# Kernel tuning notes

Measured on AMD Instinct MI355X. Metric: run time of the kernel, lower is better.

The kernel has to match this reference:

```python
import jax, jax.numpy as jnp
import numpy as np


def swiglu(g, u):
    return jax.nn.silu(g) * u


def setup_inputs() -> dict:
    key = jax.random.key(0)
    ks = jax.random.split(key, 10)
    D, H, E, HS = 2048, 512, 32, 1024
    B, S = 1, 2048
    s = 0.02
    return {
        "x": jax.random.normal(ks[0], (B, S, D), jnp.float32),
        "gate_w": jax.random.normal(ks[1], (E, D), jnp.float32) * s,
        "expert_bias": jnp.zeros((E,), jnp.float32),
        "wg": jax.random.normal(ks[2], (E, D, H), jnp.float32) * s,
        "wu": jax.random.normal(ks[3], (E, D, H), jnp.float32) * s,
        "wd": jax.random.normal(ks[4], (E, H, D), jnp.float32) * s,
        "sg": jax.random.normal(ks[5], (D, HS), jnp.float32) * s,
        "su": jax.random.normal(ks[6], (D, HS), jnp.float32) * s,
        "sd": jax.random.normal(ks[7], (HS, D), jnp.float32) * s,
        "coef_w": jax.random.normal(ks[8], (2, D), jnp.float32) * s,
        "coef_b": jnp.zeros((2,), jnp.float32),
        "top_k": 4,
    }


def reference(x, gate_w, expert_bias, wg, wu, wd, sg, su, sd, coef_w, coef_b, top_k):
    # --- sigmoid router with bias-adjusted top-k selection ---
    logits = jnp.einsum("bsd,ed->bse", x, gate_w)            # [B,S,E]
    routing = jax.nn.sigmoid(logits.astype(jnp.float32))
    biased = routing + expert_bias[None, None, :]
    _, inds = jax.lax.top_k(biased, top_k)                    # [B,S,k]
    scores = jnp.take_along_axis(routing, inds, axis=-1)      # gather UNbiased weights
    scores = scores / (jnp.sum(scores, axis=-1, keepdims=True) + 1e-20)  # norm_topk_prob
    scores = scores.astype(x.dtype)

    # --- SwitchGLU experts: dense per-expert SwiGLU, then gather top-k outputs ---
    h = jnp.einsum("bsd,edh->bseh", x, wg)                    # [B,S,E,H]
    u = jnp.einsum("bsd,edh->bseh", x, wu)
    y_all = jnp.einsum("bseh,ehd->bsed", swiglu(h, u), wd)    # [B,S,E,D]
    expert_out = jnp.take_along_axis(
        y_all, inds[..., None], axis=2)                        # [B,S,k,D]
    y_experts = jnp.sum(expert_out * scores[..., None], axis=-2)  # [B,S,D]

    # --- shared expert + learned 2-way mixing coefficient ---
    shared = swiglu(x @ sg, x @ su) @ sd                      # [B,S,D]
    coef = jax.nn.softmax(jnp.einsum("bsd,cd->bsc", x, coef_w) + coef_b, axis=-1)
    return y_experts * coef[..., :1] + shared * coef[..., 1:]
```

## Files before the change

### kernel.cpp

```cpp
#include <hip/hip_runtime.h>
#include <hip/hip_bf16.h>
#include <stdint.h>

#define S_TOK   2048
#define DMODEL  2048
#define HEXP    512
#define NEXP    32
#define HSH     1024
#define NPAIR   (S_TOK * 4)
#define NT128   96
#define NT64    160

#define M128_NT  0
#define M128_TE  1
#define M128_TP0 (1 + NT128)
#define M128_TM  (1 + 2 * NT128)
#define M64_NT   (1 + 3 * NT128)
#define M64_TE   (M64_NT + 1)
#define M64_TP0  (M64_NT + 1 + NT64)
#define M64_TM   (M64_NT + 1 + 2 * NT64)
#define META_SIZE (M64_NT + 1 + 3 * NT64)

typedef short  s16x8 __attribute__((ext_vector_type(8)));
typedef __bf16 b16x8 __attribute__((ext_vector_type(8)));
typedef float  f32x4 __attribute__((ext_vector_type(4)));

__device__ __forceinline__ f32x4 mfma16x16x32(s16x8 a, s16x8 b, f32x4 c) {
    return __builtin_amdgcn_mfma_f32_16x16x32_bf16(
        __builtin_bit_cast(b16x8, a), __builtin_bit_cast(b16x8, b), c, 0, 0, 0);
}

__device__ __forceinline__ unsigned short f2bf(float f) {
    union { float f; unsigned int u; } v; v.f = f;
    unsigned int u = v.u;
    return (unsigned short)((u + 0x7FFFu + ((u >> 16) & 1u)) >> 16);
}

__device__ __forceinline__ float bf2f(unsigned short b) {
    union { unsigned int u; float f; } v; v.u = ((unsigned int)b) << 16;
    return v.f;
}

__device__ __forceinline__ void gload16(const unsigned short* g, unsigned short* l) {
    __builtin_amdgcn_global_load_lds(
        (const __attribute__((address_space(1))) void*)(uintptr_t)g,
        (__attribute__((address_space(3))) void*)(uintptr_t)l, 16, 0, 0);
}

__global__ __launch_bounds__(256)
void router_kernel(const float* __restrict__ x, const float* __restrict__ gate_w,
                   const float* __restrict__ expert_bias,
                   const float* __restrict__ coef_w, const float* __restrict__ coef_b,
                   int* __restrict__ inds, float* __restrict__ scores,
                   float* __restrict__ coefo)
{
    const int t = blockIdx.x;
    const int tid = threadIdx.x;
    const int lane = tid & 63;
    const int wave = tid >> 6;
    const float* xr = x + (size_t)t * DMODEL;

    float xv[32];
#pragma unroll
    for (int j = 0; j < 32; ++j) xv[j] = xr[lane + 64 * j];

    __shared__ float s_logits[NEXP];
    __shared__ float s_coef[2];

    for (int i = 0; i < 8; ++i) {
        const int e = wave * 8 + i;
        const float* wr = gate_w + (size_t)e * DMODEL;
        float p = 0.f;
#pragma unroll
        for (int j = 0; j < 32; ++j) p += xv[j] * wr[lane + 64 * j];
#pragma unroll
        for (int o = 32; o > 0; o >>= 1) p += __shfl_xor(p, o);
        if (lane == 0) s_logits[e] = p;
    }
    if (wave == 0) {
        for (int c = 0; c < 2; ++c) {
            const float* wr = coef_w + (size_t)c * DMODEL;
            float p = 0.f;
#pragma unroll
            for (int j = 0; j < 32; ++j) p += xv[j] * wr[lane + 64 * j];
#pragma unroll
            for (int o = 32; o > 0; o >>= 1) p += __shfl_xor(p, o);
            if (lane == 0) s_coef[c] = p;
        }
    }
    __syncthreads();
    if (tid == 0) {
        float routing[NEXP], biased[NEXP];
        for (int e = 0; e < NEXP; ++e) {
            const float r = 1.f / (1.f + expf(-s_logits[e]));
            routing[e] = r;
            biased[e] = r + expert_bias[e];
        }
        int sel[4]; float sc[4]; float ssum = 0.f;
        for (int k = 0; k < 4; ++k) {
            int best = 0; float bv = -1e30f;
            for (int e = 0; e < NEXP; ++e)
                if (biased[e] > bv) { bv = biased[e]; best = e; }
            sel[k] = best; sc[k] = routing[best]; ssum += sc[k];
            biased[best] = -1e30f;
        }
        const float inv = 1.f / (ssum + 1e-20f);
        for (int k = 0; k < 4; ++k) {
            inds[t * 4 + k] = sel[k];
            scores[t * 4 + k] = sc[k] * inv;
        }
        const float l0 = s_coef[0] + coef_b[0];
        const float l1 = s_coef[1] + coef_b[1];
        const float m = fmaxf(l0, l1);
        const float e0 = expf(l0 - m), e1 = expf(l1 - m);
        coefo[t * 2 + 0] = e0 / (e0 + e1);
        coefo[t * 2 + 1] = e1 / (e0 + e1);
    }
}

__global__ __launch_bounds__(256)
void xcast_kernel(const float* __restrict__ x, unsigned short* __restrict__ xb)
{
    const int i = (blockIdx.x * 256 + threadIdx.x) * 4;
    const float4 v = *reinterpret_cast<const float4*>(x + i);
    ushort4 o;
    o.x = f2bf(v.x); o.y = f2bf(v.y); o.z = f2bf(v.z); o.w = f2bf(v.w);
    *reinterpret_cast<ushort4*>(xb + i) = o;
}

__global__ __launch_bounds__(256)
void tconv_kernel(const float* __restrict__ src, unsigned short* __restrict__ dst,
                  const int K, const int N)
{
    __shared__ unsigned short T[64][80];
    const size_t boff = (size_t)blockIdx.z * K * N;
    const float* s = src + boff;
    unsigned short* d = dst + boff;
    const int n0 = blockIdx.x * 64, k0 = blockIdx.y * 64;
    const int tid = threadIdx.x;

    const int n4 = (tid & 15) * 4;
    const int kr = tid >> 4;
#pragma unroll
    for (int i = 0; i < 4; ++i) {
        const int k = kr + i * 16;
        const float4 v = *reinterpret_cast<const float4*>(s + (size_t)(k0 + k) * N + n0 + n4);
        T[n4 + 0][k] = f2bf(v.x);
        T[n4 + 1][k] = f2bf(v.y);
        T[n4 + 2][k] = f2bf(v.z);
        T[n4 + 3][k] = f2bf(v.w);
    }
    __syncthreads();
    const int nw = tid >> 2;
    const int kc = (tid & 3) * 16;
    uint4* o = reinterpret_cast<uint4*>(d + (size_t)(n0 + nw) * K + k0 + kc);
    o[0] = *reinterpret_cast<const uint4*>(&T[nw][kc]);
    o[1] = *reinterpret_cast<const uint4*>(&T[nw][kc + 8]);
}

__global__ __launch_bounds__(1024)
void group_kernel(const int* __restrict__ inds, const float* __restrict__ scores,
                  int* __restrict__ meta, int* __restrict__ pair_token,
                  float* __restrict__ pair_score, int* __restrict__ tok_pos)
{
    __shared__ int cnt[NEXP];
    __shared__ int off_s[NEXP];
    __shared__ int cur[NEXP];
    const int tid = threadIdx.x;
    if (tid < NEXP) cnt[tid] = 0;
    __syncthreads();
    for (int i = tid; i < NPAIR; i += 1024) atomicAdd(&cnt[inds[i]], 1);
    __syncthreads();
    if (tid == 0) {
        int run = 0, nt1 = 0, nt2 = 0;
        for (int e = 0; e < NEXP; ++e) {
            off_s[e] = run;
            const int c = cnt[e];
            for (int m0 = 0; m0 < c; m0 += 128) {
                meta[M128_TE + nt1] = e;
                meta[M128_TP0 + nt1] = run + m0;
                meta[M128_TM + nt1] = (c - m0 < 128) ? (c - m0) : 128;
                ++nt1;
            }
            for (int m0 = 0; m0 < c; m0 += 64) {
                meta[M64_TE + nt2] = e;
                meta[M64_TP0 + nt2] = run + m0;
                meta[M64_TM + nt2] = (c - m0 < 64) ? (c - m0) : 64;
                ++nt2;
            }
            run += c;
        }
        meta[M128_NT] = nt1;
        meta[M64_NT] = nt2;
    }
    __syncthreads();
    if (tid < NEXP) cur[tid] = off_s[tid];
    __syncthreads();
    for (int i = tid; i < NPAIR; i += 1024) {
        const int e = inds[i];
        const int pos = atomicAdd(&cur[e], 1);
        pair_token[pos] = i >> 2;
        pair_score[pos] = scores[i];
        tok_pos[i] = pos;
    }
}

__global__ __launch_bounds__(256, 4)
void gateup_e_kernel(const unsigned short* __restrict__ xb,
                     const unsigned short* __restrict__ Bg_all,
                     const unsigned short* __restrict__ Bu_all,
                     unsigned short* __restrict__ act,
                     const int* __restrict__ meta, const int* __restrict__ pair_token)
{
    constexpr int NT = DMODEL / 32;
    constexpr int NB = HEXP;
    __shared__ unsigned short Al[2][128][32];
    __shared__ unsigned short Bgl[2][64][32];
    __shared__ unsigned short Bul[2][64][32];

    const int tid = threadIdx.x;
    const int lane = tid & 63;
    const int wave = tid >> 6;

    const int tt = blockIdx.y;
    if (tt >= meta[M128_NT]) return;
    const int e = meta[M128_TE + tt];
    const int p0 = meta[M128_TP0 + tt];
    const int mval = meta[M128_TM + tt];
    const size_t eoff = (size_t)e * NB * DMODEL;
    const unsigned short* Bg = Bg_all + eoff;
    const unsigned short* Bu = Bu_all + eoff;
    const int n0 = blockIdx.x * 64;

    const int sub  = lane >> 2;
    const int col8 = (lane & 3) * 8;
    const int arow0 = wave * 32 + sub;
    const int arow1 = arow0 + 16;
    int q0 = p0 + arow0; if (q0 > NPAIR - 1) q0 = NPAIR - 1;
    int q1 = p0 + arow1; if (q1 > NPAIR - 1) q1 = NPAIR - 1;
    const int tok0 = pair_token[q0];
    const int tok1 = pair_token[q1];
    const unsigned short* asrc0 = xb + (size_t)tok0 * DMODEL + col8;
    const unsigned short* asrc1 = xb + (size_t)tok1 * DMODEL + col8;
    const int brow = wave * 16 + sub;
    const unsigned short* gsrc = Bg + (size_t)(n0 + brow) * DMODEL + col8;
    const unsigned short* usrc = Bu + (size_t)(n0 + brow) * DMODEL + col8;

    auto stage = [&](int buf, int k0) {
        gload16(asrc0 + k0, &Al[buf][wave * 32][0]);
        gload16(asrc1 + k0, &Al[buf][wave * 32 + 16][0]);
        gload16(gsrc + k0, &Bgl[buf][wave * 16][0]);
        gload16(usrc + k0, &Bul[buf][wave * 16][0]);
    };

    const int wm = wave >> 1, wn = wave & 1;
    const int fr = lane & 15, fq = lane >> 4;

    const f32x4 zero4 = {0.f, 0.f, 0.f, 0.f};
    f32x4 hacc[4][2], uacc[4][2];
#pragma unroll
    for (int m = 0; m < 4; ++m)
#pragma unroll
        for (int n = 0; n < 2; ++n) { hacc[m][n] = zero4; uacc[m][n] = zero4; }

    auto compute = [&](int buf) {
        const int ko = fq * 8;
        s16x8 af[4], bg[2], bu[2];
#pragma unroll
        for (int m = 0; m < 4; ++m)
            af[m] = *reinterpret_cast<const s16x8*>(&Al[buf][wm * 64 + m * 16 + fr][ko]);
#pragma unroll
        for (int n = 0; n < 2; ++n) {
            bg[n] = *reinterpret_cast<const s16x8*>(&Bgl[buf][wn * 32 + n * 16 + fr][ko]);
            bu[n] = *reinterpret_cast<const s16x8*>(&Bul[buf][wn * 32 + n * 16 + fr][ko]);
        }
#pragma unroll
        for (int m = 0; m < 4; ++m)
#pragma unroll
            for (int n = 0; n < 2; ++n) {
                hacc[m][n] = mfma16x16x32(af[m], bg[n], hacc[m][n]);
                uacc[m][n] = mfma16x16x32(af[m], bu[n], uacc[m][n]);
            }
    };

    stage(0, 0);
    __syncthreads();
#pragma unroll 1
    for (int t = 0; t < NT; ++t) {
        const int cur = t & 1;
        if (t + 1 < NT) stage(cur ^ 1, (t + 1) * 32);
        compute(cur);
        __syncthreads();
    }

#pragma unroll
    for (int m = 0; m < 4; ++m)
#pragma unroll
        for (int n = 0; n < 2; ++n) {
            const int col = n0 + wn * 32 + n * 16 + fr;
#pragma unroll
            for (int r = 0; r < 4; ++r) {
                const int rt = wm * 64 + m * 16 + fq * 4 + r;
                if (rt < mval) {
                    const float hv = hacc[m][n][r];
                    const float a = hv / (1.f + __expf(-hv)) * uacc[m][n][r];
                    act[(size_t)(p0 + rt) * NB + col] = f2bf(a);
                }
            }
        }
}

__global__ __launch_bounds__(256, 4)
void gateup_s_kernel(const unsigned short* __restrict__ xb,
                     const unsigned short* __restrict__ Bg,
                     const unsigned short* __restrict__ Bu,
                     unsigned short* __restrict__ act)
{
    constexpr int NT = DMODEL / 32;
    constexpr int NB = HSH;
    __shared__ unsigned short Al[2][64][32];
    __shared__ unsigned short Bgl[2][64][32];
    __shared__ unsigned short Bul[2][64][32];

    const int tid = threadIdx.x;
    const int lane = tid & 63;
    const int wave = tid >> 6;
    const int p0 = blockIdx.y * 64;
    const int n0 = blockIdx.x * 64;

    const int sub  = lane >> 2;
    const int col8 = (lane & 3) * 8;
    const int arow = wave * 16 + sub;
    const unsigned short* asrc = xb + (size_t)(p0 + arow) * DMODEL + col8;
    const unsigned short* gsrc = Bg + (size_t)(n0 + arow) * DMODEL + col8;
    const unsigned short* usrc = Bu + (size_t)(n0 + arow) * DMODEL + col8;

    auto stage = [&](int buf, int k0) {
        gload16(asrc + k0, &Al[buf][wave * 16][0]);
        gload16(gsrc + k0, &Bgl[buf][wave * 16][0]);
        gload16(usrc + k0, &Bul[buf][wave * 16][0]);
    };

    const int wm = wave >> 1, wn = wave & 1;
    const int fr = lane & 15, fq = lane >> 4;

    const f32x4 zero4 = {0.f, 0.f, 0.f, 0.f};
    f32x4 hacc[2][2], uacc[2][2];
#pragma unroll
    for (int m = 0; m < 2; ++m)
#pragma unroll
        for (int n = 0; n < 2; ++n) { hacc[m][n] = zero4; uacc[m][n] = zero4; }

    auto compute = [&](int buf) {
        const int ko = fq * 8;
        s16x8 af[2], bg[2], bu[2];
#pragma unroll
        for (int m = 0; m < 2; ++m)
            af[m] = *reinterpret_cast<const s16x8*>(&Al[buf][wm * 32 + m * 16 + fr][ko]);
#pragma unroll
        for (int n = 0; n < 2; ++n) {
            bg[n] = *reinterpret_cast<const s16x8*>(&Bgl[buf][wn * 32 + n * 16 + fr][ko]);
            bu[n] = *reinterpret_cast<const s16x8*>(&Bul[buf][wn * 32 + n * 16 + fr][ko]);
        }
#pragma unroll
        for (int m = 0; m < 2; ++m)
#pragma unroll
            for (int n = 0; n < 2; ++n) {
                hacc[m][n] = mfma16x16x32(af[m], bg[n], hacc[m][n]);
                uacc[m][n] = mfma16x16x32(af[m], bu[n], uacc[m][n]);
            }
    };

    stage(0, 0);
    __syncthreads();
#pragma unroll 1
    for (int t = 0; t < NT; ++t) {
        const int cur = t & 1;
        if (t + 1 < NT) stage(cur ^ 1, (t + 1) * 32);
        compute(cur);
        __syncthreads();
    }

#pragma unroll
    for (int m = 0; m < 2; ++m)
#pragma unroll
        for (int n = 0; n < 2; ++n) {
            const int col = n0 + wn * 32 + n * 16 + fr;
#pragma unroll
            for (int r = 0; r < 4; ++r) {
                const int rt = wm * 32 + m * 16 + fq * 4 + r;
                const float hv = hacc[m][n][r];
                const float a = hv / (1.f + __expf(-hv)) * uacc[m][n][r];
                act[(size_t)(p0 + rt) * NB + col] = f2bf(a);
            }
        }
}

template <bool EXPERT, int KA>
__global__ __launch_bounds__(256, 4)
void down_kernel(const unsigned short* __restrict__ act,
                 const unsigned short* __restrict__ Bd_all,
                 float* __restrict__ out, unsigned short* __restrict__ ypair,
                 const int* __restrict__ meta, const int* __restrict__ pair_token,
                 const float* __restrict__ pair_score, const float* __restrict__ coef,
                 const int* __restrict__ tok_pos)
{
    constexpr int NT = KA / 32;
    __shared__ unsigned short Al[2][64][32];
    __shared__ unsigned short Bl[2][64][32];

    const int tid = threadIdx.x;
    const int lane = tid & 63;
    const int wave = tid >> 6;

    int p0, mval;
    const unsigned short* Bd;
    if constexpr (EXPERT) {
        const int tt = blockIdx.y;
        if (tt >= meta[M64_NT]) return;
        const int e = meta[M64_TE + tt];
        p0 = meta[M64_TP0 + tt];
        mval = meta[M64_TM + tt];
        Bd = Bd_all + (size_t)e * DMODEL * KA;
    } else {
        p0 = blockIdx.y * 64;
        mval = 64;
        Bd = Bd_all;
    }
    const int n0 = blockIdx.x * 64;

    const int sub  = lane >> 2;
    const int col8 = (lane & 3) * 8;
    const int arow = wave * 16 + sub;
    int ar = p0 + arow;
    if constexpr (EXPERT) { if (ar > NPAIR - 1) ar = NPAIR - 1; }
    const unsigned short* asrc = act + (size_t)ar * KA + col8;
    const unsigned short* bsrc = Bd + (size_t)(n0 + arow) * KA + col8;

    auto stage = [&](int buf, int k0) {
        gload16(asrc + k0, &Al[buf][wave * 16][0]);
        gload16(bsrc + k0, &Bl[buf][wave * 16][0]);
    };

    const int wm = wave >> 1, wn = wave & 1;
    const int fr = lane & 15, fq = lane >> 4;

    const f32x4 zero4 = {0.f, 0.f, 0.f, 0.f};
    f32x4 acc[2][2];
#pragma unroll
    for (int m = 0; m < 2; ++m)
#pragma unroll
        for (int n = 0; n < 2; ++n) acc[m][n] = zero4;

    auto compute = [&](int buf) {
        const int ko = fq * 8;
        s16x8 af[2], bf[2];
#pragma unroll
        for (int m = 0; m < 2; ++m)
            af[m] = *reinterpret_cast<const s16x8*>(&Al[buf][wm * 32 + m * 16 + fr][ko]);
#pragma unroll
        for (int n = 0; n < 2; ++n)
            bf[n] = *reinterpret_cast<const s16x8*>(&Bl[buf][wn * 32 + n * 16 + fr][ko]);
#pragma unroll
        for (int m = 0; m < 2; ++m)
#pragma unroll
            for (int n = 0; n < 2; ++n)
                acc[m][n] = mfma16x16x32(af[m], bf[n], acc[m][n]);
    };

    stage(0, 0);
    __syncthreads();
#pragma unroll 1
    for (int t = 0; t < NT; ++t) {
        const int cur = t & 1;
        if (t + 1 < NT) stage(cur ^ 1, (t + 1) * 32);
        compute(cur);
        __syncthreads();
    }

#pragma unroll
    for (int m = 0; m < 2; ++m)
#pragma unroll
        for (int n = 0; n < 2; ++n) {
            const int col = n0 + wn * 32 + n * 16 + fr;
#pragma unroll
            for (int r = 0; r < 4; ++r) {
                const int rt = wm * 32 + m * 16 + fq * 4 + r;
                if (rt < mval) {
                    if constexpr (EXPERT) {
                        const int p = p0 + rt;
                        const float s = pair_score[p];
                        ypair[(size_t)p * DMODEL + col] = f2bf(acc[m][n][r] * s);
                    } else {
                        const int row = p0 + rt;
                        float y4 = 0.f;
#pragma unroll
                        for (int k = 0; k < 4; ++k) {
                            const int pos = tok_pos[row * 4 + k];
                            y4 += bf2f(ypair[(size_t)pos * DMODEL + col]);
                        }
                        const float c0 = coef[row * 2 + 0];
                        const float c1 = coef[row * 2 + 1];
                        out[(size_t)row * DMODEL + col] = y4 * c0 + acc[m][n][r] * c1;
                    }
                }
            }
        }
}

extern "C" void kernel_launch(void* const* d_in, const int* in_sizes, int n_in,
                              void* d_out, int out_size, void* d_ws, size_t ws_size,
                              hipStream_t stream)
{
    const float* x           = (const float*)d_in[0];
    const float* gate_w      = (const float*)d_in[1];
    const float* expert_bias = (const float*)d_in[2];
    const float* wg          = (const float*)d_in[3];
    const float* wu          = (const float*)d_in[4];
    const float* wd          = (const float*)d_in[5];
    const float* sg          = (const float*)d_in[6];
    const float* su          = (const float*)d_in[7];
    const float* sd          = (const float*)d_in[8];
    const float* coef_w      = (const float*)d_in[9];
    const float* coef_b      = (const float*)d_in[10];
    float* out = (float*)d_out;

    char* ws = (char*)d_ws;
    size_t off = 0;
    auto take = [&](size_t bytes) {
        char* p = ws + off;
        off = (off + bytes + 255) & ~(size_t)255;
        return p;
    };
    int*   inds     = (int*)  take((size_t)S_TOK * 4 * sizeof(int));
    float* scores   = (float*)take((size_t)S_TOK * 4 * sizeof(float));
    float* coefp    = (float*)take((size_t)S_TOK * 2 * sizeof(float));
    int*   meta     = (int*)  take((size_t)META_SIZE * sizeof(int));
    int*   pair_tok = (int*)  take((size_t)NPAIR * sizeof(int));
    float* pair_sc  = (float*)take((size_t)NPAIR * sizeof(float));
    int*   tok_pos  = (int*)  take((size_t)NPAIR * sizeof(int));
    unsigned short* xb    = (unsigned short*)take((size_t)S_TOK * DMODEL * 2);
    unsigned short* act   = (unsigned short*)take((size_t)NPAIR * HEXP * 2);
    unsigned short* shact = (unsigned short*)take((size_t)S_TOK * HSH * 2);
    unsigned short* ypair = (unsigned short*)take((size_t)NPAIR * DMODEL * 2);
    unsigned short* sgb   = (unsigned short*)take((size_t)HSH * DMODEL * 2);
    unsigned short* sub_  = (unsigned short*)take((size_t)HSH * DMODEL * 2);
    unsigned short* sdb   = (unsigned short*)take((size_t)DMODEL * HSH * 2);
    unsigned short* W1    = (unsigned short*)take((size_t)NEXP * DMODEL * HEXP * 2);
    unsigned short* W2    = (unsigned short*)take((size_t)NEXP * DMODEL * HEXP * 2);
    (void)ws_size; (void)in_sizes; (void)n_in; (void)out_size;

    router_kernel<<<S_TOK, 256, 0, stream>>>(x, gate_w, expert_bias, coef_w, coef_b,
                                             inds, scores, coefp);
    xcast_kernel<<<(S_TOK * DMODEL / 4) / 256, 256, 0, stream>>>(x, xb);
    group_kernel<<<1, 1024, 0, stream>>>(inds, scores, meta, pair_tok, pair_sc, tok_pos);

    tconv_kernel<<<dim3(HSH / 64, DMODEL / 64, 1), 256, 0, stream>>>(sg, sgb, DMODEL, HSH);
    tconv_kernel<<<dim3(HSH / 64, DMODEL / 64, 1), 256, 0, stream>>>(su, sub_, DMODEL, HSH);
    tconv_kernel<<<dim3(DMODEL / 64, HSH / 64, 1), 256, 0, stream>>>(sd, sdb, HSH, DMODEL);
    tconv_kernel<<<dim3(HEXP / 64, DMODEL / 64, NEXP), 256, 0, stream>>>(wg, W1, DMODEL, HEXP);
    tconv_kernel<<<dim3(HEXP / 64, DMODEL / 64, NEXP), 256, 0, stream>>>(wu, W2, DMODEL, HEXP);

    gateup_e_kernel<<<dim3(HEXP / 64, NT128), 256, 0, stream>>>(
        xb, W1, W2, act, meta, pair_tok);
    gateup_s_kernel<<<dim3(HSH / 64, S_TOK / 64), 256, 0, stream>>>(
        xb, sgb, sub_, shact);

    tconv_kernel<<<dim3(DMODEL / 64, HEXP / 64, NEXP), 256, 0, stream>>>(wd, W1, HEXP, DMODEL);

    down_kernel<true, HEXP><<<dim3(DMODEL / 64, NT64), 256, 0, stream>>>(
        act, W1, out, ypair, meta, pair_tok, pair_sc, nullptr, tok_pos);
    down_kernel<false, HSH><<<dim3(DMODEL / 64, S_TOK / 64), 256, 0, stream>>>(
        shact, sdb, out, ypair, nullptr, nullptr, nullptr, coefp, tok_pos);
}
```

Baseline: 392.0 us.

## Fold weight transposes into GEMM grids and XOR-swizzle LDS tiles

The separate shared-expert and down-projection weight transpose/convert launches are removed. Their tiles now run as extra blocks appended to the grids of the expert and shared gate/up GEMM kernels, so conversion work overlaps GEMM blocks and launch gaps disappear. Separately, the global-to-LDS column mapping and the fragment read offset are XOR-swizzled by row so MFMA operand reads hit fewer LDS bank conflicts. The risks are larger grids with uneven block costs, and reliance on stream ordering so converted weights are ready before their consumers run.

```diff
diff --git a/kernel.cpp b/kernel.cpp
--- a/kernel.cpp
+++ b/kernel.cpp
@@ -47,6 +47,40 @@
         (__attribute__((address_space(3))) void*)(uintptr_t)l, 16, 0, 0);
 }
 
+__device__ __forceinline__ int src_col8(int lane) {
+    return 8 * ((lane & 3) ^ ((lane >> 3) & 3));
+}
+__device__ __forceinline__ int frag_ko(int fr, int fq) {
+    return 8 * (fq ^ ((fr >> 1) & 3));
+}
+
+__device__ __forceinline__ void tconv_tile(const float* __restrict__ s,
+                                           unsigned short* __restrict__ d,
+                                           const int K, const int N,
+                                           const int k0, const int n0,
+                                           unsigned short* pool)
+{
+    auto T = (unsigned short (*)[80])pool;
+    const int tid = threadIdx.x;
+    const int n4 = (tid & 15) * 4;
+    const int kr = tid >> 4;
+#pragma unroll
+    for (int i = 0; i < 4; ++i) {
+        const int k = kr + i * 16;
+        const float4 v = *reinterpret_cast<const float4*>(s + (size_t)(k0 + k) * N + n0 + n4);
+        T[n4 + 0][k] = f2bf(v.x);
+        T[n4 + 1][k] = f2bf(v.y);
+        T[n4 + 2][k] = f2bf(v.z);
+        T[n4 + 3][k] = f2bf(v.w);
+    }
+    __syncthreads();
+    const int nw = tid >> 2;
+    const int kc = (tid & 3) * 16;
+    uint4* o = reinterpret_cast<uint4*>(d + (size_t)(n0 + nw) * K + k0 + kc);
+    o[0] = *reinterpret_cast<const uint4*>(&T[nw][kc]);
+    o[1] = *reinterpret_cast<const uint4*>(&T[nw][kc + 8]);
+}
+
 __global__ __launch_bounds__(256)
 void router_kernel(const float* __restrict__ x, const float* __restrict__ gate_w,
                    const float* __restrict__ expert_bias,
@@ -132,30 +166,9 @@
 void tconv_kernel(const float* __restrict__ src, unsigned short* __restrict__ dst,
                   const int K, const int N)
 {
-    __shared__ unsigned short T[64][80];
+    __shared__ unsigned short pool[64 * 80];
     const size_t boff = (size_t)blockIdx.z * K * N;
-    const float* s = src + boff;
-    unsigned short* d = dst + boff;
-    const int n0 = blockIdx.x * 64, k0 = blockIdx.y * 64;
-    const int tid = threadIdx.x;
-
-    const int n4 = (tid & 15) * 4;
-    const int kr = tid >> 4;
-#pragma unroll
-    for (int i = 0; i < 4; ++i) {
-        const int k = kr + i * 16;
-        const float4 v = *reinterpret_cast<const float4*>(s + (size_t)(k0 + k) * N + n0 + n4);
-        T[n4 + 0][k] = f2bf(v.x);
-        T[n4 + 1][k] = f2bf(v.y);
-        T[n4 + 2][k] = f2bf(v.z);
-        T[n4 + 3][k] = f2bf(v.w);
-    }
-    __syncthreads();
-    const int nw = tid >> 2;
-    const int kc = (tid & 3) * 16;
-    uint4* o = reinterpret_cast<uint4*>(d + (size_t)(n0 + nw) * K + k0 + kc);
-    o[0] = *reinterpret_cast<const uint4*>(&T[nw][kc]);
-    o[1] = *reinterpret_cast<const uint4*>(&T[nw][kc + 8]);
+    tconv_tile(src + boff, dst + boff, K, N, blockIdx.y * 64, blockIdx.x * 64, pool);
 }
 
 __global__ __launch_bounds__(1024)
@@ -210,17 +223,32 @@
                      const unsigned short* __restrict__ Bg_all,
                      const unsigned short* __restrict__ Bu_all,
                      unsigned short* __restrict__ act,
-                     const int* __restrict__ meta, const int* __restrict__ pair_token)
+                     const int* __restrict__ meta, const int* __restrict__ pair_token,
+                     const float* __restrict__ sg, const float* __restrict__ su,
+                     const float* __restrict__ sd,
+                     unsigned short* __restrict__ sgb, unsigned short* __restrict__ sub_,
+                     unsigned short* __restrict__ sdb)
 {
     constexpr int NT = DMODEL / 32;
     constexpr int NB = HEXP;
-    __shared__ unsigned short Al[2][128][32];
-    __shared__ unsigned short Bgl[2][64][32];
-    __shared__ unsigned short Bul[2][64][32];
+    __shared__ unsigned short pool[16384];
+    auto Al  = (unsigned short (*)[128][32])(pool);
+    auto Bgl = (unsigned short (*)[64][32])(pool + 8192);
+    auto Bul = (unsigned short (*)[64][32])(pool + 12288);
 
     const int tid = threadIdx.x;
     const int lane = tid & 63;
     const int wave = tid >> 6;
+
+    if (blockIdx.y >= NT128) {
+        const int tile = (blockIdx.y - NT128) * 8 + blockIdx.x;
+        const int which = tile / 512;
+        const int t = tile % 512;
+        if (which == 0)      tconv_tile(sg, sgb, DMODEL, HSH, (t >> 4) * 64, (t & 15) * 64, pool);
+        else if (which == 1) tconv_tile(su, sub_, DMODEL, HSH, (t >> 4) * 64, (t & 15) * 64, pool);
+        else                 tconv_tile(sd, sdb, HSH, DMODEL, (t >> 5) * 64, (t & 31) * 64, pool);
+        return;
+    }
 
     const int tt = blockIdx.y;
     if (tt >= meta[M128_NT]) return;
@@ -233,7 +261,7 @@
     const int n0 = blockIdx.x * 64;
 
     const int sub  = lane >> 2;
-    const int col8 = (lane & 3) * 8;
+    const int col8 = src_col8(lane);
     const int arow0 = wave * 32 + sub;
     const int arow1 = arow0 + 16;
     int q0 = p0 + arow0; if (q0 > NPAIR - 1) q0 = NPAIR - 1;
@@ -255,6 +283,7 @@
 
     const int wm = wave >> 1, wn = wave & 1;
     const int fr = lane & 15, fq = lane >> 4;
+    const int ko = frag_ko(fr, fq);
 
     const f32x4 zero4 = {0.f, 0.f, 0.f, 0.f};
     f32x4 hacc[4][2], uacc[4][2];
@@ -264,7 +293,6 @@
         for (int n = 0; n < 2; ++n) { hacc[m][n] = zero4; uacc[m][n] = zero4; }
 
     auto compute = [&](int buf) {
-        const int ko = fq * 8;
         s16x8 af[4], bg[2], bu[2];
 #pragma unroll
         for (int m = 0; m < 4; ++m)
@@ -314,22 +342,34 @@
 void gateup_s_kernel(const unsigned short* __restrict__ xb,
                      const unsigned short* __restrict__ Bg,
                      const unsigned short* __restrict__ Bu,
-                     unsigned short* __restrict__ act)
+                     unsigned short* __restrict__ act,
+                     const float* __restrict__ wd, unsigned short* __restrict__ wdb)
 {
     constexpr int NT = DMODEL / 32;
     constexpr int NB = HSH;
-    __shared__ unsigned short Al[2][64][32];
-    __shared__ unsigned short Bgl[2][64][32];
-    __shared__ unsigned short Bul[2][64][32];
+    __shared__ unsigned short pool[12288];
+    auto Al  = (unsigned short (*)[64][32])(pool);
+    auto Bgl = (unsigned short (*)[64][32])(pool + 4096);
+    auto Bul = (unsigned short (*)[64][32])(pool + 8192);
 
     const int tid = threadIdx.x;
     const int lane = tid & 63;
     const int wave = tid >> 6;
+
+    if (blockIdx.y >= S_TOK / 64) {
+        const int tile = (blockIdx.y - S_TOK / 64) * 16 + blockIdx.x;
+        const int e = tile >> 8;
+        const int t = tile & 255;
+        tconv_tile(wd + (size_t)e * HEXP * DMODEL, wdb + (size_t)e * DMODEL * HEXP,
+                   HEXP, DMODEL, (t >> 5) * 64, (t & 31) * 64, pool);
+        return;
+    }
+
     const int p0 = blockIdx.y * 64;
     const int n0 = blockIdx.x * 64;
 
     const int sub  = lane >> 2;
-    const int col8 = (lane & 3) * 8;
+    const int col8 = src_col8(lane);
     const int arow = wave * 16 + sub;
     const unsigned short* asrc = xb + (size_t)(p0 + arow) * DMODEL + col8;
     const unsigned short* gsrc = Bg + (size_t)(n0 + arow) * DMODEL + col8;
@@ -343,6 +383,7 @@
 
     const int wm = wave >> 1, wn = wave & 1;
     const int fr = lane & 15, fq = lane >> 4;
+    const int ko = frag_ko(fr, fq);
 
     const f32x4 zero4 = {0.f, 0.f, 0.f, 0.f};
     f32x4 hacc[2][2], uacc[2][2];
@@ -352,7 +393,6 @@
         for (int n = 0; n < 2; ++n) { hacc[m][n] = zero4; uacc[m][n] = zero4; }
 
     auto compute = [&](int buf) {
-        const int ko = fq * 8;
         s16x8 af[2], bg[2], bu[2];
 #pragma unroll
         for (int m = 0; m < 2; ++m)
@@ -430,7 +470,7 @@
     const int n0 = blockIdx.x * 64;
 
     const int sub  = lane >> 2;
-    const int col8 = (lane & 3) * 8;
+    const int col8 = src_col8(lane);
     const int arow = wave * 16 + sub;
     int ar = p0 + arow;
     if constexpr (EXPERT) { if (ar > NPAIR - 1) ar = NPAIR - 1; }
@@ -444,6 +484,7 @@
 
     const int wm = wave >> 1, wn = wave & 1;
     const int fr = lane & 15, fq = lane >> 4;
+    const int ko = frag_ko(fr, fq);
 
     const f32x4 zero4 = {0.f, 0.f, 0.f, 0.f};
     f32x4 acc[2][2];
@@ -453,7 +494,6 @@
         for (int n = 0; n < 2; ++n) acc[m][n] = zero4;
 
     auto compute = [&](int buf) {
-        const int ko = fq * 8;
         s16x8 af[2], bf[2];
 #pragma unroll
         for (int m = 0; m < 2; ++m)
@@ -555,18 +595,13 @@
     xcast_kernel<<<(S_TOK * DMODEL / 4) / 256, 256, 0, stream>>>(x, xb);
     group_kernel<<<1, 1024, 0, stream>>>(inds, scores, meta, pair_tok, pair_sc, tok_pos);
 
-    tconv_kernel<<<dim3(HSH / 64, DMODEL / 64, 1), 256, 0, stream>>>(sg, sgb, DMODEL, HSH);
-    tconv_kernel<<<dim3(HSH / 64, DMODEL / 64, 1), 256, 0, stream>>>(su, sub_, DMODEL, HSH);
-    tconv_kernel<<<dim3(DMODEL / 64, HSH / 64, 1), 256, 0, stream>>>(sd, sdb, HSH, DMODEL);
     tconv_kernel<<<dim3(HEXP / 64, DMODEL / 64, NEXP), 256, 0, stream>>>(wg, W1, DMODEL, HEXP);
     tconv_kernel<<<dim3(HEXP / 64, DMODEL / 64, NEXP), 256, 0, stream>>>(wu, W2, DMODEL, HEXP);
 
-    gateup_e_kernel<<<dim3(HEXP / 64, NT128), 256, 0, stream>>>(
-        xb, W1, W2, act, meta, pair_tok);
-    gateup_s_kernel<<<dim3(HSH / 64, S_TOK / 64), 256, 0, stream>>>(
-        xb, sgb, sub_, shact);
-
-    tconv_kernel<<<dim3(DMODEL / 64, HEXP / 64, NEXP), 256, 0, stream>>>(wd, W1, HEXP, DMODEL);
+    gateup_e_kernel<<<dim3(HEXP / 64, NT128 + 192), 256, 0, stream>>>(
+        xb, W1, W2, act, meta, pair_tok, sg, su, sd, sgb, sub_, sdb);
+    gateup_s_kernel<<<dim3(HSH / 64, S_TOK / 64 + 512), 256, 0, stream>>>(
+        xb, sgb, sub_, shact, wd, W1);
 
     down_kernel<true, HEXP><<<dim3(DMODEL / 64, NT64), 256, 0, stream>>>(
         act, W1, out, ypair, meta, pair_tok, pair_sc, nullptr, tok_pos);
```

Measured after the change: 362.1 us. 7.6% less time.
